# Kernel tuning notes

Hardware: AMD Instinct MI355X
Metric: run time of the kernel (lower is better)

Reference implementation:

```python
import jax, jax.numpy as jnp
import numpy as np

N = 100000          # nodes
DEG = 16            # fixed in-degree -> E = N*DEG edges
E = N * DEG
NEG_SLOPE = 0.2
HEADS = 4
HID = 64            # per-head hidden dim; layer width = HEADS*HID = 256
IN_DIM = 256
NUM_CLASSES = 41


def setup_inputs() -> dict:
    key = jax.random.key(0)
    ks = jax.random.split(key, 12)
    # CSC-style structure: for destination node i, col_ind[row_ptr[i]:row_ptr[i+1]] are its source neighbors
    row_ptr = (jnp.arange(N + 1, dtype=jnp.int32) * DEG)
    col_ind = jax.random.randint(ks[0], (E,), 0, N, dtype=jnp.int32)
    inputs = jax.random.normal(ks[1], (N, IN_DIM), dtype=jnp.float32)

    def glorot(k, shape):
        fan = sum(shape)
        return jax.random.normal(k, shape, dtype=jnp.float32) * jnp.sqrt(2.0 / fan)

    W0 = glorot(ks[2], (IN_DIM, HEADS * HID))
    al0 = glorot(ks[3], (HEADS, HID)); ar0 = glorot(ks[4], (HEADS, HID))
    W1 = glorot(ks[5], (HEADS * HID, HEADS * HID))
    al1 = glorot(ks[6], (HEADS, HID)); ar1 = glorot(ks[7], (HEADS, HID))
    W2 = glorot(ks[8], (HEADS * HID, HEADS * NUM_CLASSES))
    al2 = glorot(ks[9], (HEADS, NUM_CLASSES)); ar2 = glorot(ks[10], (HEADS, NUM_CLASSES))
    return {"row_ptr": row_ptr, "col_ind": col_ind, "inputs": inputs,
            "W0": W0, "al0": al0, "ar0": ar0,
            "W1": W1, "al1": al1, "ar1": ar1,
            "W2": W2, "al2": al2, "ar2": ar2}


def _gat_conv(h, W, a_l, a_r, src, dst, out_dim):
    # h: [N, F_in] -> feat: [N, H, D]
    feat = (h @ W).reshape(N, HEADS, out_dim)
    el = jnp.einsum('nhd,hd->nh', feat, a_l)   # [N, H] source-side score
    er = jnp.einsum('nhd,hd->nh', feat, a_r)   # [N, H] dest-side score
    e = jax.nn.leaky_relu(el[src] + er[dst], NEG_SLOPE)  # [E, H]
    # edge softmax over incoming edges of each destination node
    emax = jax.ops.segment_max(e, dst, num_segments=N)
    ex = jnp.exp(e - emax[dst])
    denom = jax.ops.segment_sum(ex, dst, num_segments=N)
    alpha = ex / denom[dst]                     # [E, H]
    # attention-weighted aggregation of source features
    msg = alpha[:, :, None] * feat[src]         # [E, H, D]
    return jax.ops.segment_sum(msg, dst, num_segments=N)  # [N, H, D]


def reference(row_ptr, col_ind, inputs, W0, al0, ar0, W1, al1, ar1, W2, al2, ar2):
    deg = jnp.diff(row_ptr)
    dst = jnp.repeat(jnp.arange(N, dtype=jnp.int32), deg, total_repeat_length=E)
    src = col_ind
    h = _gat_conv(inputs, W0, al0, ar0, src, dst, HID).reshape(N, HEADS * HID)
    h = _gat_conv(h, W1, al1, ar1, src, dst, HID).reshape(N, HEADS * HID)
    logits = _gat_conv(h, W2, al2, ar2, src, dst, NUM_CLASSES).mean(axis=1)  # [N, C]
    return logits
```

## Files before the change

kernel.cpp:

```cpp
#include <hip/hip_runtime.h>

#define NN 100000
#define DEG 16
#define HEADS 4
#define NEG_SLOPE 0.2f
#define NPAD 100096

typedef unsigned short ushort_t;
typedef __attribute__((ext_vector_type(8))) short bf16x8;
typedef __attribute__((ext_vector_type(4))) float f32x4;

__device__ __forceinline__ ushort_t f2bf_rn(float f) {
    uint32_t u = __float_as_uint(f);
    uint32_t r = (u + 0x7fffu + ((u >> 16) & 1u)) >> 16;
    return (ushort_t)r;
}
__device__ __forceinline__ float bf2f(ushort_t u) {
    return __uint_as_float(((uint32_t)u) << 16);
}

__device__ __forceinline__ void gld16(const void* g, void* l) {
    __builtin_amdgcn_global_load_lds(
        (const __attribute__((address_space(1))) unsigned int*)g,
        (__attribute__((address_space(3))) unsigned int*)l, 16, 0, 0);
}

__global__ __launch_bounds__(256) void prep_wt(
    const float* __restrict__ W, ushort_t* __restrict__ Wh,
    ushort_t* __restrict__ Wl, int ncr)
{
    int idx = blockIdx.x * 256 + threadIdx.x;
    int j     = idx & 7;
    int chunk = idx >> 3;
    int ln   = chunk & 63;
    int nf   = (chunk >> 6) & 3;
    int ksub = (chunk >> 8) & 1;
    int wn   = (chunk >> 9) & 1;
    int k0g  = (chunk >> 10) & 3;
    int p    = (chunk >> 12) & 1;
    int col = p * 128 + wn * 64 + nf * 16 + (ln & 15);
    int k   = k0g * 64 + ksub * 32 + (ln >> 4) * 8 + j;
    float v = (col < ncr) ? W[k * ncr + col] : 0.f;
    uint32_t b  = __float_as_uint(v);
    uint32_t hb = b & 0xffff0000u;
    float r = v - __uint_as_float(hb);
    Wh[idx] = (ushort_t)(hb >> 16);
    Wl[idx] = (ushort_t)(__float_as_uint(r) >> 16);
}

template <int AMODE, bool DO_SCORES>
__global__ __launch_bounds__(256) void gemm_mfma(
    const float* __restrict__ A32,
    const ushort_t* __restrict__ Ahi, const ushort_t* __restrict__ Alo,
    const ushort_t* __restrict__ Bth, const ushort_t* __restrict__ Btl,
    const float* __restrict__ al, const float* __restrict__ ar,
    ushort_t* __restrict__ Cb, int ldc, int ncr,
    float* __restrict__ el, float* __restrict__ er)
{
    __shared__ uint4 smem[2048];
    __shared__ uint4 smemB[2048];

    const int tid  = threadIdx.x;
    const int wv   = tid >> 6;
    const int ln   = tid & 63;
    const int wm   = wv >> 1;
    const int wn   = wv & 1;
    const int cl   = ln & 15;
    const int kq   = ln >> 4;
    const int row0 = blockIdx.y * 128;
    const int col0 = blockIdx.x * 128;

    const ushort_t* bH = Bth + (size_t)blockIdx.x * 4 * 8192;
    const ushort_t* bL = Btl + (size_t)blockIdx.x * 4 * 8192;

    f32x4 acc[4][4] = {};

    for (int k0g = 0; k0g < 4; ++k0g) {
        const int k0 = k0g * 64;
        if (k0) __syncthreads();

        {
            const ushort_t* rh = bH + k0g * 8192;
            const ushort_t* rl = bL + k0g * 8192;
            #pragma unroll
            for (int q = 0; q < 4; ++q) {
                int i = wv * 4 + q;
                gld16(rh + (size_t)(i * 64 + ln) * 8, (char*)smemB + i * 1024);
                gld16(rl + (size_t)(i * 64 + ln) * 8, (char*)smemB + 16384 + i * 1024);
            }
        }

        if (AMODE == 1) {
            const int rl8 = ln >> 3;
            const int c   = (ln & 7) ^ rl8;
            #pragma unroll
            for (int q = 0; q < 4; ++q) {
                int rb = wv * 4 + q;
                size_t g = (size_t)(row0 + rb * 8 + rl8) * 256 + k0 + c * 8;
                gld16(Ahi + g, (char*)smem + rb * 1024);
                gld16(Alo + g, (char*)smem + 16384 + rb * 1024);
            }
        } else {
            #pragma unroll
            for (int p = 0; p < 4; ++p) {
                int s = p * 256 + tid;
                int row = s >> 3, c = s & 7;
                int csw = c ^ (row & 7);
                int gr = row0 + row;
                float4 v0 = make_float4(0.f,0.f,0.f,0.f), v1 = v0;
                if (gr < NN) {
                    const float* g = A32 + (size_t)gr * 256 + k0 + c * 8;
                    v0 = *reinterpret_cast<const float4*>(g);
                    v1 = *reinterpret_cast<const float4*>(g + 4);
                }
                uint32_t b0 = __float_as_uint(v0.x), b1 = __float_as_uint(v0.y);
                uint32_t b2 = __float_as_uint(v0.z), b3 = __float_as_uint(v0.w);
                uint32_t b4 = __float_as_uint(v1.x), b5 = __float_as_uint(v1.y);
                uint32_t b6 = __float_as_uint(v1.z), b7 = __float_as_uint(v1.w);
                uint4 vh;
                vh.x = (b1 & 0xffff0000u) | (b0 >> 16);
                vh.y = (b3 & 0xffff0000u) | (b2 >> 16);
                vh.z = (b5 & 0xffff0000u) | (b4 >> 16);
                vh.w = (b7 & 0xffff0000u) | (b6 >> 16);
                float r0 = v0.x - __uint_as_float(b0 & 0xffff0000u);
                float r1 = v0.y - __uint_as_float(b1 & 0xffff0000u);
                float r2 = v0.z - __uint_as_float(b2 & 0xffff0000u);
                float r3 = v0.w - __uint_as_float(b3 & 0xffff0000u);
                float r4 = v1.x - __uint_as_float(b4 & 0xffff0000u);
                float r5 = v1.y - __uint_as_float(b5 & 0xffff0000u);
                float r6 = v1.z - __uint_as_float(b6 & 0xffff0000u);
                float r7 = v1.w - __uint_as_float(b7 & 0xffff0000u);
                uint4 vl;
                vl.x = (__float_as_uint(r1) & 0xffff0000u) | (__float_as_uint(r0) >> 16);
                vl.y = (__float_as_uint(r3) & 0xffff0000u) | (__float_as_uint(r2) >> 16);
                vl.z = (__float_as_uint(r5) & 0xffff0000u) | (__float_as_uint(r4) >> 16);
                vl.w = (__float_as_uint(r7) & 0xffff0000u) | (__float_as_uint(r6) >> 16);
                smem[row * 8 + csw]        = vh;
                smem[1024 + row * 8 + csw] = vl;
            }
        }
        __syncthreads();

        #pragma unroll
        for (int ksub = 0; ksub < 2; ++ksub) {
            bf16x8 ah[4], ax[4];
            #pragma unroll
            for (int mf = 0; mf < 4; ++mf) {
                int row = wm * 64 + mf * 16 + cl;
                int chunk = (ksub * 4 + kq) ^ (row & 7);
                int idx = row * 8 + chunk;
                ah[mf] = ((const bf16x8*)smem)[idx];
                ax[mf] = ((const bf16x8*)smem)[1024 + idx];
            }
            #pragma unroll
            for (int nf = 0; nf < 4; ++nf) {
                int bidx = ((wn * 2 + ksub) * 4 + nf) * 64 + ln;
                bf16x8 bh = ((const bf16x8*)smemB)[bidx];
                bf16x8 bl = ((const bf16x8*)smemB)[1024 + bidx];
                #pragma unroll
                for (int mf = 0; mf < 4; ++mf) {
                    acc[mf][nf] = __builtin_amdgcn_mfma_f32_16x16x32_bf16(ah[mf], bh, acc[mf][nf], 0, 0, 0);
                    acc[mf][nf] = __builtin_amdgcn_mfma_f32_16x16x32_bf16(ah[mf], bl, acc[mf][nf], 0, 0, 0);
                    acc[mf][nf] = __builtin_amdgcn_mfma_f32_16x16x32_bf16(ax[mf], bh, acc[mf][nf], 0, 0, 0);
                }
            }
        }
    }

    #pragma unroll
    for (int mf = 0; mf < 4; ++mf) {
        int gr0 = row0 + wm * 64 + mf * 16 + kq * 4;
        #pragma unroll
        for (int r = 0; r < 4; ++r) {
            int gr = gr0 + r;
            if (gr < NN) {
                #pragma unroll
                for (int nf = 0; nf < 4; ++nf) {
                    int gc = col0 + wn * 64 + nf * 16 + cl;
                    if (gc < ncr)
                        Cb[(size_t)gr * ldc + gc] = f2bf_rn(acc[mf][nf][r]);
                }
            }
        }
    }

    if (DO_SCORES) {
        const int head = blockIdx.x * 2 + wn;
        float alv[4], arv[4];
        #pragma unroll
        for (int nf = 0; nf < 4; ++nf) {
            int d = nf * 16 + cl;
            alv[nf] = al[head * 64 + d];
            arv[nf] = ar[head * 64 + d];
        }
        #pragma unroll
        for (int mf = 0; mf < 4; ++mf) {
            #pragma unroll
            for (int r = 0; r < 4; ++r) {
                float pl = 0.f, pr = 0.f;
                #pragma unroll
                for (int nf = 0; nf < 4; ++nf) {
                    pl += acc[mf][nf][r] * alv[nf];
                    pr += acc[mf][nf][r] * arv[nf];
                }
                #pragma unroll
                for (int msk = 1; msk <= 8; msk <<= 1) {
                    pl += __shfl_xor(pl, msk);
                    pr += __shfl_xor(pr, msk);
                }
                if (cl == 0) {
                    int gr = row0 + wm * 64 + mf * 16 + kq * 4 + r;
                    if (gr < NN) {
                        el[gr * HEADS + head] = pl;
                        er[gr * HEADS + head] = pr;
                    }
                }
            }
        }
    }
}

__global__ __launch_bounds__(256) void scores2_bf(
    const ushort_t* __restrict__ featb, const float* __restrict__ al,
    const float* __restrict__ ar, float* __restrict__ el, float* __restrict__ er)
{
    const int n = blockIdx.x;
    const int t = threadIdx.x;
    const int h = t >> 6;
    const int j = t & 63;
    float v = 0.f, u = 0.f;
    if (j < 41) {
        float f = bf2f(featb[(size_t)n * 164 + h * 41 + j]);
        v = f * al[h * 41 + j];
        u = f * ar[h * 41 + j];
    }
    #pragma unroll
    for (int off = 32; off > 0; off >>= 1) {
        v += __shfl_down(v, off);
        u += __shfl_down(u, off);
    }
    if (j == 0) {
        el[n * HEADS + h] = v;
        er[n * HEADS + h] = u;
    }
}

__global__ __launch_bounds__(256) void agg_full_bf(
    const ushort_t* __restrict__ featb, const float* __restrict__ el,
    const float* __restrict__ er, const int* __restrict__ col,
    ushort_t* __restrict__ Hhi, ushort_t* __restrict__ Hlo)
{
    __shared__ int   s_src[4][DEG];
    __shared__ float s_alpha[4][HEADS][DEG];

    const int t = threadIdx.x;
    const int w = t >> 6;
    const int l = t & 63;
    const int n = blockIdx.x * 4 + w;
    const int h = l >> 4;
    const int k = l & 15;

    const int src_k = col[n * DEG + k];
    float x = el[src_k * HEADS + h] + er[n * HEADS + h];
    x = x > 0.f ? x : NEG_SLOPE * x;

    float m = x;
    #pragma unroll
    for (int msk = 8; msk >= 1; msk >>= 1) m = fmaxf(m, __shfl_xor(m, msk));
    float ex = __expf(x - m);
    float s = ex;
    #pragma unroll
    for (int msk = 8; msk >= 1; msk >>= 1) s += __shfl_xor(s, msk);

    s_alpha[w][h][k] = ex / s;
    if (l < DEG) s_src[w][l] = src_k;
    __syncthreads();

    float4 acc = make_float4(0.f, 0.f, 0.f, 0.f);
    #pragma unroll
    for (int k2 = 0; k2 < DEG; ++k2) {
        const int   sk = s_src[w][k2];
        const float a  = s_alpha[w][h][k2];
        ushort4 f = *reinterpret_cast<const ushort4*>(&featb[(size_t)sk * 256 + l * 4]);
        acc.x += a * bf2f(f.x);
        acc.y += a * bf2f(f.y);
        acc.z += a * bf2f(f.z);
        acc.w += a * bf2f(f.w);
    }
    uint32_t bx = __float_as_uint(acc.x), by = __float_as_uint(acc.y);
    uint32_t bz = __float_as_uint(acc.z), bw = __float_as_uint(acc.w);
    ushort4 hv;
    hv.x = (ushort_t)(bx >> 16); hv.y = (ushort_t)(by >> 16);
    hv.z = (ushort_t)(bz >> 16); hv.w = (ushort_t)(bw >> 16);
    float rx = acc.x - __uint_as_float(bx & 0xffff0000u);
    float ry = acc.y - __uint_as_float(by & 0xffff0000u);
    float rz = acc.z - __uint_as_float(bz & 0xffff0000u);
    float rw = acc.w - __uint_as_float(bw & 0xffff0000u);
    ushort4 lv;
    lv.x = (ushort_t)(__float_as_uint(rx) >> 16);
    lv.y = (ushort_t)(__float_as_uint(ry) >> 16);
    lv.z = (ushort_t)(__float_as_uint(rz) >> 16);
    lv.w = (ushort_t)(__float_as_uint(rw) >> 16);
    *reinterpret_cast<ushort4*>(&Hhi[(size_t)n * 256 + l * 4]) = hv;
    *reinterpret_cast<ushort4*>(&Hlo[(size_t)n * 256 + l * 4]) = lv;
}

__global__ __launch_bounds__(256) void agg_out_bf(
    const ushort_t* __restrict__ featb, const float* __restrict__ el,
    const float* __restrict__ er, const int* __restrict__ col,
    float* __restrict__ out)
{
    __shared__ int   s_src[4][DEG];
    __shared__ float s_alpha[4][HEADS][DEG];
    __shared__ float s_agg[4][164];

    const int t = threadIdx.x;
    const int w = t >> 6;
    const int l = t & 63;
    const int n = blockIdx.x * 4 + w;
    const int h = l >> 4;
    const int k = l & 15;

    const int src_k = col[n * DEG + k];
    float x = el[src_k * HEADS + h] + er[n * HEADS + h];
    x = x > 0.f ? x : NEG_SLOPE * x;

    float m = x;
    #pragma unroll
    for (int msk = 8; msk >= 1; msk >>= 1) m = fmaxf(m, __shfl_xor(m, msk));
    float ex = __expf(x - m);
    float s = ex;
    #pragma unroll
    for (int msk = 8; msk >= 1; msk >>= 1) s += __shfl_xor(s, msk);

    s_alpha[w][h][k] = ex / s;
    if (l < DEG) s_src[w][l] = src_k;
    __syncthreads();

    const int l41 = l < 41 ? l : 40;
    const int c0 = 4 * l41;
    const int h0 = (c0 + 0) / 41, h1 = (c0 + 1) / 41;
    const int h2 = (c0 + 2) / 41, h3 = (c0 + 3) / 41;

    float4 acc = make_float4(0.f, 0.f, 0.f, 0.f);
    #pragma unroll
    for (int k2 = 0; k2 < DEG; ++k2) {
        const int sk = s_src[w][k2];
        ushort4 f = *reinterpret_cast<const ushort4*>(&featb[(size_t)sk * 164 + c0]);
        acc.x += s_alpha[w][h0][k2] * bf2f(f.x);
        acc.y += s_alpha[w][h1][k2] * bf2f(f.y);
        acc.z += s_alpha[w][h2][k2] * bf2f(f.z);
        acc.w += s_alpha[w][h3][k2] * bf2f(f.w);
    }
    if (l < 41) *reinterpret_cast<float4*>(&s_agg[w][c0]) = acc;
    __syncthreads();
    if (l < 41)
        out[(size_t)n * 41 + l] =
            0.25f * (s_agg[w][l] + s_agg[w][l + 41] + s_agg[w][l + 82] + s_agg[w][l + 123]);
}

extern "C" void kernel_launch(void* const* d_in, const int* in_sizes, int n_in,
                              void* d_out, int out_size, void* d_ws, size_t ws_size,
                              hipStream_t stream)
{
    const int*   col_ind = (const int*)  d_in[1];
    const float* inputs  = (const float*)d_in[2];
    const float* W0      = (const float*)d_in[3];
    const float* al0     = (const float*)d_in[4];
    const float* ar0     = (const float*)d_in[5];
    const float* W1      = (const float*)d_in[6];
    const float* al1     = (const float*)d_in[7];
    const float* ar1     = (const float*)d_in[8];
    const float* W2      = (const float*)d_in[9];
    const float* al2     = (const float*)d_in[10];
    const float* ar2     = (const float*)d_in[11];
    float* out = (float*)d_out;

    char* ws = (char*)d_ws;
    const size_t seg = (size_t)NPAD * 256 * sizeof(ushort_t);
    ushort_t* h_hi  = (ushort_t*)(ws);
    ushort_t* h_lo  = (ushort_t*)(ws + seg);
    ushort_t* featb = (ushort_t*)(ws + 2 * seg);
    float*    el    = (float*)(ws + 3 * seg);
    float*    er    = el + (size_t)NN * HEADS;
    ushort_t* wt    = (ushort_t*)(er + (size_t)NN * HEADS);
    ushort_t* wt0h = wt;              ushort_t* wt0l = wt + 65536;
    ushort_t* wt1h = wt + 2 * 65536;  ushort_t* wt1l = wt + 3 * 65536;
    ushort_t* wt2h = wt + 4 * 65536;  ushort_t* wt2l = wt + 5 * 65536;

    dim3 blk(256);
    dim3 gg(2, (NN + 127) / 128);
    const int waveGrid = NN / 4;

    prep_wt<<<256, blk, 0, stream>>>(W0, wt0h, wt0l, 256);
    prep_wt<<<256, blk, 0, stream>>>(W1, wt1h, wt1l, 256);
    prep_wt<<<256, blk, 0, stream>>>(W2, wt2h, wt2l, 164);

    gemm_mfma<0, true><<<gg, blk, 0, stream>>>(
        inputs, nullptr, nullptr, wt0h, wt0l, al0, ar0, featb, 256, 256, el, er);
    agg_full_bf<<<waveGrid, blk, 0, stream>>>(featb, el, er, col_ind, h_hi, h_lo);

    gemm_mfma<1, true><<<gg, blk, 0, stream>>>(
        nullptr, h_hi, h_lo, wt1h, wt1l, al1, ar1, featb, 256, 256, el, er);
    agg_full_bf<<<waveGrid, blk, 0, stream>>>(featb, el, er, col_ind, h_hi, h_lo);

    gemm_mfma<1, false><<<gg, blk, 0, stream>>>(
        nullptr, h_hi, h_lo, wt2h, wt2l, nullptr, nullptr, featb, 164, 164, nullptr, nullptr);
    scores2_bf<<<NN, blk, 0, stream>>>(featb, al2, ar2, el, er);
    agg_out_bf<<<waveGrid, blk, 0, stream>>>(featb, el, er, col_ind, out);
}
```

Baseline: 646.5 us.

## Slice hidden features by 32-column chunks and split softmax from aggregation

The GEMM now writes layer-0/1 features in a column-sliced layout, with 8 slices of 32 bf16 columns stored contiguously per node. Aggregation runs one block per (32-node group, slice), so each gathered neighbour row slice is 64 bytes and the working set per pass is smaller and more cache-friendly. Edge softmax moves into a separate alpha_prep kernel that packs the source index and a 15-bit quantized alpha into one uint32 per edge per head. This adds a kernel launch and an extra per-edge buffer round trip, and quantizing alpha to 15 bits loses some precision.

```diff
diff --git a/kernel.cpp b/kernel.cpp
--- a/kernel.cpp
+++ b/kernel.cpp
@@ -48,7 +48,7 @@
     Wl[idx] = (ushort_t)(__float_as_uint(r) >> 16);
 }
 
-template <int AMODE, bool DO_SCORES>
+template <int AMODE, bool DO_SCORES, bool SLICED>
 __global__ __launch_bounds__(256) void gemm_mfma(
     const float* __restrict__ A32,
     const ushort_t* __restrict__ Ahi, const ushort_t* __restrict__ Alo,
@@ -177,8 +177,12 @@
                 #pragma unroll
                 for (int nf = 0; nf < 4; ++nf) {
                     int gc = col0 + wn * 64 + nf * 16 + cl;
-                    if (gc < ncr)
-                        Cb[(size_t)gr * ldc + gc] = f2bf_rn(acc[mf][nf][r]);
+                    if (gc < ncr) {
+                        if (SLICED)
+                            Cb[((size_t)(gc >> 5) * NPAD + gr) * 32 + (gc & 31)] = f2bf_rn(acc[mf][nf][r]);
+                        else
+                            Cb[(size_t)gr * ldc + gc] = f2bf_rn(acc[mf][nf][r]);
+                    }
                 }
             }
         }
@@ -220,39 +224,10 @@
     }
 }
 
-__global__ __launch_bounds__(256) void scores2_bf(
-    const ushort_t* __restrict__ featb, const float* __restrict__ al,
-    const float* __restrict__ ar, float* __restrict__ el, float* __restrict__ er)
-{
-    const int n = blockIdx.x;
-    const int t = threadIdx.x;
-    const int h = t >> 6;
-    const int j = t & 63;
-    float v = 0.f, u = 0.f;
-    if (j < 41) {
-        float f = bf2f(featb[(size_t)n * 164 + h * 41 + j]);
-        v = f * al[h * 41 + j];
-        u = f * ar[h * 41 + j];
-    }
-    #pragma unroll
-    for (int off = 32; off > 0; off >>= 1) {
-        v += __shfl_down(v, off);
-        u += __shfl_down(u, off);
-    }
-    if (j == 0) {
-        el[n * HEADS + h] = v;
-        er[n * HEADS + h] = u;
-    }
-}
-
-__global__ __launch_bounds__(256) void agg_full_bf(
-    const ushort_t* __restrict__ featb, const float* __restrict__ el,
-    const float* __restrict__ er, const int* __restrict__ col,
-    ushort_t* __restrict__ Hhi, ushort_t* __restrict__ Hlo)
-{
-    __shared__ int   s_src[4][DEG];
-    __shared__ float s_alpha[4][HEADS][DEG];
-
+__global__ __launch_bounds__(256) void alpha_prep(
+    const float* __restrict__ el, const float* __restrict__ er,
+    const int* __restrict__ col, uint32_t* __restrict__ srcalpha)
+{
     const int t = threadIdx.x;
     const int w = t >> 6;
     const int l = t & 63;
@@ -260,8 +235,8 @@
     const int h = l >> 4;
     const int k = l & 15;
 
-    const int src_k = col[n * DEG + k];
-    float x = el[src_k * HEADS + h] + er[n * HEADS + h];
+    const int src = col[n * DEG + k];
+    float x = el[src * HEADS + h] + er[n * HEADS + h];
     x = x > 0.f ? x : NEG_SLOPE * x;
 
     float m = x;
@@ -272,21 +247,46 @@
     #pragma unroll
     for (int msk = 8; msk >= 1; msk >>= 1) s += __shfl_xor(s, msk);
 
-    s_alpha[w][h][k] = ex / s;
-    if (l < DEG) s_src[w][l] = src_k;
+    uint32_t aq = (uint32_t)(ex / s * 32767.f + 0.5f);
+    if (aq > 32767u) aq = 32767u;
+    srcalpha[(size_t)n * 64 + l] = ((uint32_t)src << 15) | aq;
+}
+
+__global__ __launch_bounds__(256) void agg_sliced(
+    const ushort_t* __restrict__ fsl,
+    const uint32_t* __restrict__ srcalpha,
+    ushort_t* __restrict__ Hhi, ushort_t* __restrict__ Hlo)
+{
+    __shared__ uint32_t s_pack[32][17];
+
+    const int bid = blockIdx.x;
+    const int s = bid & 7;
+    const int g = bid >> 3;
+    const int t = threadIdx.x;
+    const int nl = t >> 3;
+    const int j  = t & 7;
+    const int n  = g * 32 + nl;
+    const int h  = s >> 1;
+
+    uint2 e2 = *reinterpret_cast<const uint2*>(
+        &srcalpha[(size_t)n * 64 + h * 16 + j * 2]);
+    s_pack[nl][j * 2]     = e2.x;
+    s_pack[nl][j * 2 + 1] = e2.y;
     __syncthreads();
 
+    const ushort_t* base = fsl + (size_t)s * NPAD * 32 + j * 4;
     float4 acc = make_float4(0.f, 0.f, 0.f, 0.f);
     #pragma unroll
-    for (int k2 = 0; k2 < DEG; ++k2) {
-        const int   sk = s_src[w][k2];
-        const float a  = s_alpha[w][h][k2];
-        ushort4 f = *reinterpret_cast<const ushort4*>(&featb[(size_t)sk * 256 + l * 4]);
+    for (int k = 0; k < DEG; ++k) {
+        const uint32_t e = s_pack[nl][k];
+        const float a = (float)(e & 0x7fffu) * (1.f / 32767.f);
+        ushort4 f = *reinterpret_cast<const ushort4*>(&base[(size_t)(e >> 15) * 32]);
         acc.x += a * bf2f(f.x);
         acc.y += a * bf2f(f.y);
         acc.z += a * bf2f(f.z);
         acc.w += a * bf2f(f.w);
     }
+
     uint32_t bx = __float_as_uint(acc.x), by = __float_as_uint(acc.y);
     uint32_t bz = __float_as_uint(acc.z), bw = __float_as_uint(acc.w);
     ushort4 hv;
@@ -301,8 +301,34 @@
     lv.y = (ushort_t)(__float_as_uint(ry) >> 16);
     lv.z = (ushort_t)(__float_as_uint(rz) >> 16);
     lv.w = (ushort_t)(__float_as_uint(rw) >> 16);
-    *reinterpret_cast<ushort4*>(&Hhi[(size_t)n * 256 + l * 4]) = hv;
-    *reinterpret_cast<ushort4*>(&Hlo[(size_t)n * 256 + l * 4]) = lv;
+    const size_t o = (size_t)n * 256 + s * 32 + j * 4;
+    *reinterpret_cast<ushort4*>(&Hhi[o]) = hv;
+    *reinterpret_cast<ushort4*>(&Hlo[o]) = lv;
+}
+
+__global__ __launch_bounds__(256) void scores2_bf(
+    const ushort_t* __restrict__ featb, const float* __restrict__ al,
+    const float* __restrict__ ar, float* __restrict__ el, float* __restrict__ er)
+{
+    const int n = blockIdx.x;
+    const int t = threadIdx.x;
+    const int h = t >> 6;
+    const int j = t & 63;
+    float v = 0.f, u = 0.f;
+    if (j < 41) {
+        float f = bf2f(featb[(size_t)n * 164 + h * 41 + j]);
+        v = f * al[h * 41 + j];
+        u = f * ar[h * 41 + j];
+    }
+    #pragma unroll
+    for (int off = 32; off > 0; off >>= 1) {
+        v += __shfl_down(v, off);
+        u += __shfl_down(u, off);
+    }
+    if (j == 0) {
+        el[n * HEADS + h] = v;
+        er[n * HEADS + h] = u;
+    }
 }
 
 __global__ __launch_bounds__(256) void agg_out_bf(
@@ -381,7 +407,8 @@
     ushort_t* h_hi  = (ushort_t*)(ws);
     ushort_t* h_lo  = (ushort_t*)(ws + seg);
     ushort_t* featb = (ushort_t*)(ws + 2 * seg);
-    float*    el    = (float*)(ws + 3 * seg);
+    uint32_t* salph = (uint32_t*)(ws + 3 * seg);
+    float*    el    = (float*)(ws + 3 * seg + (size_t)NN * 64 * 4);
     float*    er    = el + (size_t)NN * HEADS;
     ushort_t* wt    = (ushort_t*)(er + (size_t)NN * HEADS);
     ushort_t* wt0h = wt;              ushort_t* wt0l = wt + 65536;
@@ -390,22 +417,25 @@
 
     dim3 blk(256);
     dim3 gg(2, (NN + 127) / 128);
-    const int waveGrid = NN / 4;
+    const int nodeGrid = NN / 4;
+    const int sliceGrid = (NN / 32) * 8;
 
     prep_wt<<<256, blk, 0, stream>>>(W0, wt0h, wt0l, 256);
     prep_wt<<<256, blk, 0, stream>>>(W1, wt1h, wt1l, 256);
     prep_wt<<<256, blk, 0, stream>>>(W2, wt2h, wt2l, 164);
 
-    gemm_mfma<0, true><<<gg, blk, 0, stream>>>(
+    gemm_mfma<0, true, true><<<gg, blk, 0, stream>>>(
         inputs, nullptr, nullptr, wt0h, wt0l, al0, ar0, featb, 256, 256, el, er);
-    agg_full_bf<<<waveGrid, blk, 0, stream>>>(featb, el, er, col_ind, h_hi, h_lo);
-
-    gemm_mfma<1, true><<<gg, blk, 0, stream>>>(
+    alpha_prep<<<nodeGrid, blk, 0, stream>>>(el, er, col_ind, salph);
+    agg_sliced<<<sliceGrid, blk, 0, stream>>>(featb, salph, h_hi, h_lo);
+
+    gemm_mfma<1, true, true><<<gg, blk, 0, stream>>>(
         nullptr, h_hi, h_lo, wt1h, wt1l, al1, ar1, featb, 256, 256, el, er);
-    agg_full_bf<<<waveGrid, blk, 0, stream>>>(featb, el, er, col_ind, h_hi, h_lo);
-
-    gemm_mfma<1, false><<<gg, blk, 0, stream>>>(
+    alpha_prep<<<nodeGrid, blk, 0, stream>>>(el, er, col_ind, salph);
+    agg_sliced<<<sliceGrid, blk, 0, stream>>>(featb, salph, h_hi, h_lo);
+
+    gemm_mfma<1, false, false><<<gg, blk, 0, stream>>>(
         nullptr, h_hi, h_lo, wt2h, wt2l, nullptr, nullptr, featb, 164, 164, nullptr, nullptr);
     scores2_bf<<<NN, blk, 0, stream>>>(featb, al2, ar2, el, er);
-    agg_out_bf<<<waveGrid, blk, 0, stream>>>(featb, el, er, col_ind, out);
-}
+    agg_out_bf<<<nodeGrid, blk, 0, stream>>>(featb, el, er, col_ind, out);
+}
```

After: 686.8 us. +6.2%, slower.
